# Kernel optimization log

Hardware: AMD Instinct MI355X
Metric: run time of the kernel (lower is better)

Reference implementation:

```python
import jax, jax.numpy as jnp
import numpy as np

N = 50000      # total nodes
E = 600000     # edges
F_IN = 128     # dataset.num_features
G = 500        # graphs (100 nodes each)
K = 30         # sort-pool k
D1, D2, D3 = 64, 64, 1
DTOT = D1 + D2 + D3  # 129


def gcn_conv(x, W, b, src, dst, dinv, n):
    # PyG GCNConv: x' = D^-1/2 (A+I) D^-1/2 (x W) + b ; src/dst include self-loops
    h = x @ W
    norm = dinv[src] * dinv[dst]
    msg = h[src] * norm[:, None]
    return jax.ops.segment_sum(msg, dst, num_segments=n) + b


def setup_inputs():
    key = jax.random.key(0)
    ks = jax.random.split(key, 24)
    rn = lambda k, s, sc=0.1: jax.random.normal(k, s, dtype=jnp.float32) * sc
    return {
        "x": jax.random.normal(ks[0], (N, F_IN), dtype=jnp.float32),
        "edge_index": jax.random.randint(ks[1], (2, E), 0, N),
        "W1": rn(ks[2], (F_IN, D1)), "b1": rn(ks[3], (D1,)),
        "W2": rn(ks[4], (D1, D2)),  "b2": rn(ks[5], (D2,)),
        "W3": rn(ks[6], (D2, D3)),  "b3": rn(ks[7], (D3,)),
        "Ws1": rn(ks[8], (D1, 1)),  "bs1": rn(ks[9], (1,)),
        "Ws2": rn(ks[10], (D2, 1)), "bs2": rn(ks[11], (1,)),
        "Ws3": rn(ks[12], (D3, 1)), "bs3": rn(ks[13], (1,)),
        "Wc1": rn(ks[14], (16, 1, DTOT)), "bc1": rn(ks[15], (16,)),
        "Wc2": rn(ks[16], (32, 16, 5)),   "bc2": rn(ks[17], (32,)),
        "Wl1": rn(ks[18], (128, 352)),    "bl1": rn(ks[19], (128,)),
        "Wl2": rn(ks[20], (1, 128)),      "bl2": rn(ks[21], (1,)),
        "num_graphs": G,
    }


def reference(x, edge_index, W1, b1, W2, b2, W3, b3, Ws1, bs1, Ws2, bs2, Ws3, bs3,
              Wc1, bc1, Wc2, bc2, Wl1, bl1, Wl2, bl2, num_graphs):
    n = x.shape[0]
    loops = jnp.arange(n)
    src = jnp.concatenate([edge_index[0], loops])
    dst = jnp.concatenate([edge_index[1], loops])
    deg = jnp.zeros((n,), jnp.float32).at[dst].add(1.0)
    dinv = jnp.where(deg > 0, deg ** -0.5, 0.0)

    h = jax.nn.relu(gcn_conv(x, W1, b1, src, dst, dinv, n))
    x1 = gcn_conv(h, Ws1, bs1, src, dst, dinv, n) * h
    h = jax.nn.relu(gcn_conv(h, W2, b2, src, dst, dinv, n))
    x2 = gcn_conv(h, Ws2, bs2, src, dst, dinv, n) * h
    h = jax.nn.relu(gcn_conv(h, W3, b3, src, dst, dinv, n))
    x3 = gcn_conv(h, Ws3, bs3, src, dst, dinv, n) * h
    feats = jnp.concatenate([x1, x2, x3], axis=1)  # [N, 129]

    # global_sort_pool: equal-size graphs (batch = id // npg), sort desc by last channel, keep top-K
    npg = n // num_graphs
    fg = feats.reshape(num_graphs, npg, DTOT)
    order = jnp.argsort(-fg[:, :, -1], axis=1)[:, :K]                 # [G, K]
    pooled = jnp.take_along_axis(fg, order[:, :, None], axis=1)       # [G, K, 129]

    # Conv1d(1->16, kernel=129, stride=129) == per-position dense over the 129-dim blocks
    c1 = jax.nn.relu(jnp.einsum('gkd,cd->gck', pooled, Wc1[:, 0, :]) + bc1[None, :, None])  # [G,16,30]
    mp = c1.reshape(num_graphs, 16, K // 2, 2).max(axis=-1)           # MaxPool1d(2,2) -> [G,16,15]
    c2 = jax.lax.conv_general_dilated(mp, Wc2, window_strides=(1,), padding='VALID',
                                      dimension_numbers=('NCH', 'OIH', 'NCH')) + bc2[None, :, None]
    c2 = jax.nn.relu(c2)                                              # [G,32,11]
    flat = c2.reshape(num_graphs, -1)                                 # [G,352]
    hdd = jax.nn.relu(flat @ Wl1.T + bl1)
    out = hdd @ Wl2.T + bl2
    return out[:, 0]
```

## Files before the change

kernel.cpp:

```cpp
#include <hip/hip_runtime.h>
#include <hip/hip_bf16.h>

#define NN 50000
#define EE 600000
#define FIN 128
#define GG 500
#define NPG 100
#define KK 30
#define SCHUNK 1024

__global__ void psg_deg(const int* __restrict__ dst, int* __restrict__ deg, int e) {
    int i = blockIdx.x * blockDim.x + threadIdx.x;
    if (i < e) atomicAdd(&deg[dst[i]], 1);
}

__global__ __launch_bounds__(SCHUNK) void psg_scan1(const int* __restrict__ deg,
                                                    int* __restrict__ rowptr,
                                                    int* __restrict__ csums,
                                                    float* __restrict__ dinv, int n) {
    __shared__ int sm[SCHUNK];
    int t = threadIdx.x;
    int base = blockIdx.x * SCHUNK;
    int v = (base + t < n) ? deg[base + t] : 0;
    sm[t] = v;
    __syncthreads();
    for (int off = 1; off < SCHUNK; off <<= 1) {
        int u = (t >= off) ? sm[t - off] : 0;
        __syncthreads();
        sm[t] += u;
        __syncthreads();
    }
    if (base + t < n) {
        rowptr[base + t] = sm[t] - v;
        dinv[base + t] = 1.0f / sqrtf((float)(v + 1));
    }
    if (t == SCHUNK - 1) csums[blockIdx.x] = sm[t];
}

__global__ __launch_bounds__(SCHUNK) void psg_scan3(int* __restrict__ rowptr,
                                                    int* __restrict__ rowfill,
                                                    const int* __restrict__ csums,
                                                    int n, int e) {
    __shared__ int soff;
    int t = threadIdx.x;
    if (t < 64) {
        int c = (t < (int)blockIdx.x) ? csums[t] : 0;
#pragma unroll
        for (int o = 1; o < 64; o <<= 1) c += __shfl_xor(c, o, 64);
        if (t == 0) soff = c;
    }
    __syncthreads();
    int i = blockIdx.x * SCHUNK + t;
    if (i < n) {
        int v = rowptr[i] + soff;
        rowptr[i] = v;
        rowfill[i] = v;
    }
    if (i == 0) rowptr[n] = e;
}

__global__ void psg_build(const int* __restrict__ src, const int* __restrict__ dst,
                          int* __restrict__ rowfill, int* __restrict__ csr_src, int e) {
    int i = blockIdx.x * blockDim.x + threadIdx.x;
    if (i < e) {
        int pos = atomicAdd(&rowfill[dst[i]], 1);
        csr_src[pos] = src[i];
    }
}

template <int KD>
__global__ __launch_bounds__(256) void psg_gemm(const float* __restrict__ X,
                                                const float* __restrict__ W,
                                                const float* __restrict__ dinv,
                                                float* __restrict__ hs, int n) {
    __shared__ __align__(16) float Xl[16][KD];
    __shared__ __align__(16) float WtF[(KD / 4) * 64 * 4];
    int t = threadIdx.x;
    int r0 = blockIdx.x * 16;
    for (int i = t; i < KD * 64; i += 256) {
        int k = i >> 6, j = i & 63;
        WtF[(((k >> 2) * 64 + j) << 2) + (k & 3)] = W[i];
    }
    for (int i4 = t; i4 < 16 * (KD / 4); i4 += 256) {
        int r = i4 / (KD / 4), u = i4 % (KD / 4);
        int row = r0 + r;
        float4 v = make_float4(0.f, 0.f, 0.f, 0.f);
        if (row < n) v = ((const float4*)(X + (size_t)row * KD))[u];
        ((float4*)&Xl[r][0])[u] = v;
    }
    __syncthreads();
    int j = t & 63, q = t >> 6;
    const float4* Wt4 = (const float4*)WtF;
    float a0 = 0.f, a1 = 0.f, a2 = 0.f, a3 = 0.f;
#pragma unroll 4
    for (int u = 0; u < KD / 4; ++u) {
        float4 wv = Wt4[u * 64 + j];
        float4 x0 = *(const float4*)&Xl[q * 4 + 0][u * 4];
        float4 x1 = *(const float4*)&Xl[q * 4 + 1][u * 4];
        float4 x2 = *(const float4*)&Xl[q * 4 + 2][u * 4];
        float4 x3 = *(const float4*)&Xl[q * 4 + 3][u * 4];
        a0 += x0.x * wv.x + x0.y * wv.y + x0.z * wv.z + x0.w * wv.w;
        a1 += x1.x * wv.x + x1.y * wv.y + x1.z * wv.z + x1.w * wv.w;
        a2 += x2.x * wv.x + x2.y * wv.y + x2.z * wv.z + x2.w * wv.w;
        a3 += x3.x * wv.x + x3.y * wv.y + x3.z * wv.z + x3.w * wv.w;
    }
    float av[4] = {a0, a1, a2, a3};
#pragma unroll
    for (int rr = 0; rr < 4; rr++) {
        int row = r0 + q * 4 + rr;
        if (row < n) hs[(size_t)row * 64 + j] = av[rr] * dinv[row];
    }
}

template <int NDOT>
__global__ __launch_bounds__(256) void psg_gfin(const float* __restrict__ hs,
                                                const int* __restrict__ rowptr,
                                                const int* __restrict__ csr_src,
                                                const float* __restrict__ dinv,
                                                const float* __restrict__ b,
                                                float* __restrict__ h,
                                                const float* __restrict__ wv0,
                                                float* __restrict__ s0_src,
                                                const float* __restrict__ wv1,
                                                float* __restrict__ s1_src, int n) {
    int w = (int)((blockIdx.x * 256 + threadIdx.x) >> 6);
    int j = threadIdx.x & 63;
    if (w >= n) return;
    int p0 = rowptr[w], p1 = rowptr[w + 1];
    float a0 = hs[(size_t)w * 64 + j];
    float a1 = 0.f, a2 = 0.f, a3 = 0.f, a4 = 0.f, a5 = 0.f, a6 = 0.f, a7 = 0.f;
    int p = p0;
    for (; p + 8 <= p1; p += 8) {
        int s0 = csr_src[p],     s1 = csr_src[p + 1], s2 = csr_src[p + 2], s3 = csr_src[p + 3];
        int s4 = csr_src[p + 4], s5 = csr_src[p + 5], s6 = csr_src[p + 6], s7 = csr_src[p + 7];
        a0 += hs[(size_t)s0 * 64 + j];
        a1 += hs[(size_t)s1 * 64 + j];
        a2 += hs[(size_t)s2 * 64 + j];
        a3 += hs[(size_t)s3 * 64 + j];
        a4 += hs[(size_t)s4 * 64 + j];
        a5 += hs[(size_t)s5 * 64 + j];
        a6 += hs[(size_t)s6 * 64 + j];
        a7 += hs[(size_t)s7 * 64 + j];
    }
    if (p + 4 <= p1) {
        int s0 = csr_src[p], s1 = csr_src[p + 1], s2 = csr_src[p + 2], s3 = csr_src[p + 3];
        a4 += hs[(size_t)s0 * 64 + j];
        a5 += hs[(size_t)s1 * 64 + j];
        a6 += hs[(size_t)s2 * 64 + j];
        a7 += hs[(size_t)s3 * 64 + j];
        p += 4;
    }
    for (; p < p1; ++p) a1 += hs[(size_t)csr_src[p] * 64 + j];
    float a = ((a0 + a1) + (a2 + a3)) + ((a4 + a5) + (a6 + a7));
    float di = dinv[w];
    float v = fmaxf(a * di + b[j], 0.f);
    h[(size_t)w * 64 + j] = v;
    float t0 = v * wv0[j];
#pragma unroll
    for (int o = 32; o; o >>= 1) t0 += __shfl_xor(t0, o, 64);
    if (j == 0) s0_src[w] = t0 * di;
    if (NDOT == 2) {
        float t1 = v * wv1[j];
#pragma unroll
        for (int o = 32; o; o >>= 1) t1 += __shfl_xor(t1, o, 64);
        if (j == 0) s1_src[w] = t1 * di;
    }
}

__global__ void psg_h3g(const float* __restrict__ sc_src,
                        const int* __restrict__ rowptr, const int* __restrict__ csr_src,
                        const float* __restrict__ dinv, const float* __restrict__ b3,
                        const float* __restrict__ Ws3,
                        float* __restrict__ h3, float* __restrict__ u_src, int n) {
    int i = blockIdx.x * blockDim.x + threadIdx.x;
    if (i < n) {
        float a = sc_src[i];
        int p1 = rowptr[i + 1];
        for (int p = rowptr[i]; p < p1; ++p) a += sc_src[csr_src[p]];
        float di = dinv[i];
        float v = fmaxf(a * di + b3[0], 0.f);
        h3[i] = v;
        u_src[i] = v * Ws3[0] * di;
    }
}

__device__ __forceinline__ int psg_f2ord(float f) {
    int s = __float_as_int(f);
    return s < 0 ? (s ^ 0x7fffffff) : s;
}

__global__ __launch_bounds__(128) void psg_spcnn(const float* __restrict__ u_src,
                                                 const int* __restrict__ rowptr,
                                                 const int* __restrict__ csr_src,
                                                 const float* __restrict__ dinv,
                                                 const float* __restrict__ bs1,
                                                 const float* __restrict__ bs2,
                                                 const float* __restrict__ bs3,
                                                 const float* __restrict__ sA_src,
                                                 const float* __restrict__ sB_src,
                                                 const float* __restrict__ h1,
                                                 const float* __restrict__ h2,
                                                 const float* __restrict__ h3,
                                                 const float* __restrict__ Wc1, const float* __restrict__ bc1,
                                                 const float* __restrict__ Wc2, const float* __restrict__ bc2,
                                                 const float* __restrict__ Wl1, const float* __restrict__ bl1,
                                                 const float* __restrict__ Wl2, const float* __restrict__ bl2,
                                                 float* __restrict__ out) {
    int g = blockIdx.x, t = threadIdx.x;
    __shared__ float pl[KK * 129];
    __shared__ float wc1l[16 * 129];
    __shared__ float wc2l[32 * 16 * 5];
    __shared__ float key[NPG];
    __shared__ int ord[NPG];
    __shared__ int sel[KK];
    __shared__ float sa[KK], sb[KK];
    __shared__ float c1[16 * KK];
    __shared__ float mp[16 * 15];
    __shared__ float c2s[352];
    __shared__ float hdds[128];
    __shared__ float red[2];
    for (int i = t; i < 16 * 129; i += 128) wc1l[i] = Wc1[i];
    for (int i = t; i < 32 * 16 * 5; i += 128) wc2l[i] = Wc2[i];
    if (t < NPG) {
        int node = g * NPG + t;
        float a = u_src[node];
        int pe = rowptr[node + 1];
        for (int p = rowptr[node]; p < pe; ++p) a += u_src[csr_src[p]];
        float v = (a * dinv[node] + bs3[0]) * h3[node];
        key[t] = v;
        ord[t] = psg_f2ord(v);
    }
    __syncthreads();
    if (t < NPG) {
        int v = ord[t];
        int r = 0;
        for (int m = 0; m < NPG; m++) {
            int u = ord[m];
            r += (u > v) || (u == v && m < t);
        }
        if (r < KK) sel[r] = t;
    }
    __syncthreads();
    {
        int r = t & 31;
        if (t < 64 && r < KK) {
            int node = g * NPG + sel[r];
            const float* ssrc = (t < 32) ? sA_src : sB_src;
            float a = ssrc[node];
            int pe = rowptr[node + 1];
            for (int p = rowptr[node]; p < pe; ++p) a += ssrc[csr_src[p]];
            float scl = a * dinv[node] + ((t < 32) ? bs1[0] : bs2[0]);
            if (t < 32) sa[r] = scl; else sb[r] = scl;
        }
    }
    __syncthreads();
    for (int idx = t; idx < KK * 129; idx += 128) {
        int r = idx / 129, c = idx - r * 129;
        int node = g * NPG + sel[r];
        float v;
        if (c < 64) v = sa[r] * h1[(size_t)node * 64 + c];
        else if (c < 128) v = sb[r] * h2[(size_t)node * 64 + (c - 64)];
        else v = key[sel[r]];
        pl[idx] = v;
    }
    __syncthreads();
    for (int idx = t; idx < 16 * KK; idx += 128) {
        int c = idx / KK, k = idx % KK;
        float a = bc1[c];
        for (int d = 0; d < 129; d++) a += pl[k * 129 + d] * wc1l[c * 129 + d];
        c1[c * KK + k] = fmaxf(a, 0.f);
    }
    __syncthreads();
    for (int idx = t; idx < 16 * 15; idx += 128) {
        int c = idx / 15, k = idx % 15;
        mp[idx] = fmaxf(c1[c * KK + 2 * k], c1[c * KK + 2 * k + 1]);
    }
    __syncthreads();
    for (int idx = t; idx < 352; idx += 128) {
        int o = idx / 11, k = idx % 11;
        float a = bc2[o];
        for (int i2 = 0; i2 < 16; i2++) {
#pragma unroll
            for (int k2 = 0; k2 < 5; k2++) a += mp[i2 * 15 + k + k2] * wc2l[(o * 16 + i2) * 5 + k2];
        }
        c2s[o * 11 + k] = fmaxf(a, 0.f);
    }
    __syncthreads();
    {
        float a = bl1[t];
        const float* wr = Wl1 + (size_t)t * 352;
        for (int f = 0; f < 352; f++) a += c2s[f] * wr[f];
        hdds[t] = fmaxf(a, 0.f);
    }
    __syncthreads();
    float p = hdds[t] * Wl2[t];
#pragma unroll
    for (int o = 32; o; o >>= 1) p += __shfl_xor(p, o, 64);
    if ((t & 63) == 0) red[t >> 6] = p;
    __syncthreads();
    if (t == 0) out[g] = red[0] + red[1] + bl2[0];
}

extern "C" void kernel_launch(void* const* d_in, const int* in_sizes, int n_in,
                              void* d_out, int out_size, void* d_ws, size_t ws_size,
                              hipStream_t stream) {
    const float* x   = (const float*)d_in[0];
    const int*   ei  = (const int*)d_in[1];
    const float* W1  = (const float*)d_in[2];
    const float* b1  = (const float*)d_in[3];
    const float* W2  = (const float*)d_in[4];
    const float* b2  = (const float*)d_in[5];
    const float* W3  = (const float*)d_in[6];
    const float* b3  = (const float*)d_in[7];
    const float* Ws1 = (const float*)d_in[8];
    const float* bs1 = (const float*)d_in[9];
    const float* Ws2 = (const float*)d_in[10];
    const float* bs2 = (const float*)d_in[11];
    const float* Ws3 = (const float*)d_in[12];
    const float* bs3 = (const float*)d_in[13];
    const float* Wc1 = (const float*)d_in[14];
    const float* bc1 = (const float*)d_in[15];
    const float* Wc2 = (const float*)d_in[16];
    const float* bc2 = (const float*)d_in[17];
    const float* Wl1 = (const float*)d_in[18];
    const float* bl1 = (const float*)d_in[19];
    const float* Wl2 = (const float*)d_in[20];
    const float* bl2 = (const float*)d_in[21];
    float* out = (float*)d_out;

    const int n = in_sizes[0] / FIN;
    const int e = in_sizes[1] / 2;
    const int* src = ei;
    const int* dst = ei + e;
    const int nchunk = (n + SCHUNK - 1) / SCHUNK;

    char* w = (char*)d_ws;
    float* dinv    = (float*)w; w += (size_t)n * 4;
    float* sA_src  = (float*)w; w += (size_t)n * 4;
    float* sB_src  = (float*)w; w += (size_t)n * 4;
    float* sC_src  = (float*)w; w += (size_t)n * 4;
    float* h3      = (float*)w; w += (size_t)n * 4;
    float* u_src   = (float*)w; w += (size_t)n * 4;
    int*   deg     = (int*)w;   w += (size_t)n * 4;
    int*   rowptr  = (int*)w;   w += (size_t)(n + 1) * 4;
    int*   rowfill = (int*)w;   w += (size_t)n * 4;
    int*   csums   = (int*)w;   w += 64 * 4;
    int*   csr_src = (int*)w;   w += (size_t)e * 4;
    float* hs      = (float*)w; w += (size_t)n * 64 * 4;
    float* h1      = (float*)w; w += (size_t)n * 64 * 4;
    float* h2      = (float*)w; w += (size_t)n * 64 * 4;

    const int nb_e  = (e + 255) / 256;
    const int nb_n  = (n + 255) / 256;
    const int nb_g  = (n + 15) / 16;
    const int nb_nw = (n * 64 + 255) / 256;

    hipMemsetAsync(deg, 0, (size_t)n * 4, stream);
    psg_deg<<<nb_e, 256, 0, stream>>>(dst, deg, e);
    psg_scan1<<<nchunk, SCHUNK, 0, stream>>>(deg, rowptr, csums, dinv, n);
    psg_scan3<<<nchunk, SCHUNK, 0, stream>>>(rowptr, rowfill, csums, n, e);
    psg_build<<<nb_e, 256, 0, stream>>>(src, dst, rowfill, csr_src, e);

    psg_gemm<128><<<nb_g, 256, 0, stream>>>(x, W1, dinv, hs, n);
    psg_gfin<1><<<nb_nw, 256, 0, stream>>>(hs, rowptr, csr_src, dinv, b1, h1,
                                           Ws1, sA_src, nullptr, nullptr, n);

    psg_gemm<64><<<nb_g, 256, 0, stream>>>(h1, W2, dinv, hs, n);
    psg_gfin<2><<<nb_nw, 256, 0, stream>>>(hs, rowptr, csr_src, dinv, b2, h2,
                                           Ws2, sB_src, W3, sC_src, n);

    psg_h3g<<<nb_n, 256, 0, stream>>>(sC_src, rowptr, csr_src, dinv, b3, Ws3, h3, u_src, n);

    psg_spcnn<<<GG, 128, 0, stream>>>(u_src, rowptr, csr_src, dinv, bs1, bs2, bs3,
                                      sA_src, sB_src, h1, h2, h3,
                                      Wc1, bc1, Wc2, bc2, Wl1, bl1, Wl2, bl2, out);

    (void)n_in; (void)out_size; (void)ws_size;
}
```

Before: 346.2 us.

## Move per-node scalar gathers out of sort-pool kernel into full-grid passes

```diff
diff --git a/kernel.cpp b/kernel.cpp
--- a/kernel.cpp
+++ b/kernel.cpp
@@ -167,20 +167,44 @@
     }
 }
 
-__global__ void psg_h3g(const float* __restrict__ sc_src,
+__global__ void psg_h3g(const float* __restrict__ sC_src,
+                        const float* __restrict__ sA_src,
+                        const float* __restrict__ sB_src,
                         const int* __restrict__ rowptr, const int* __restrict__ csr_src,
                         const float* __restrict__ dinv, const float* __restrict__ b3,
                         const float* __restrict__ Ws3,
-                        float* __restrict__ h3, float* __restrict__ u_src, int n) {
+                        const float* __restrict__ bs1, const float* __restrict__ bs2,
+                        float* __restrict__ h3, float* __restrict__ u_src,
+                        float* __restrict__ xs1, float* __restrict__ xs2, int n) {
     int i = blockIdx.x * blockDim.x + threadIdx.x;
     if (i < n) {
-        float a = sc_src[i];
+        float aC = sC_src[i], aA = sA_src[i], aB = sB_src[i];
         int p1 = rowptr[i + 1];
-        for (int p = rowptr[i]; p < p1; ++p) a += sc_src[csr_src[p]];
+        for (int p = rowptr[i]; p < p1; ++p) {
+            int s = csr_src[p];
+            aC += sC_src[s];
+            aA += sA_src[s];
+            aB += sB_src[s];
+        }
         float di = dinv[i];
-        float v = fmaxf(a * di + b3[0], 0.f);
+        float v = fmaxf(aC * di + b3[0], 0.f);
         h3[i] = v;
         u_src[i] = v * Ws3[0] * di;
+        xs1[i] = aA * di + bs1[0];
+        xs2[i] = aB * di + bs2[0];
+    }
+}
+
+__global__ void psg_x3g(const float* __restrict__ u_src,
+                        const int* __restrict__ rowptr, const int* __restrict__ csr_src,
+                        const float* __restrict__ dinv, const float* __restrict__ bs3,
+                        const float* __restrict__ h3, float* __restrict__ x3, int n) {
+    int i = blockIdx.x * blockDim.x + threadIdx.x;
+    if (i < n) {
+        float a = u_src[i];
+        int p1 = rowptr[i + 1];
+        for (int p = rowptr[i]; p < p1; ++p) a += u_src[csr_src[p]];
+        x3[i] = (a * dinv[i] + bs3[0]) * h3[i];
     }
 }
 
@@ -189,18 +213,11 @@
     return s < 0 ? (s ^ 0x7fffffff) : s;
 }
 
-__global__ __launch_bounds__(128) void psg_spcnn(const float* __restrict__ u_src,
-                                                 const int* __restrict__ rowptr,
-                                                 const int* __restrict__ csr_src,
-                                                 const float* __restrict__ dinv,
-                                                 const float* __restrict__ bs1,
-                                                 const float* __restrict__ bs2,
-                                                 const float* __restrict__ bs3,
-                                                 const float* __restrict__ sA_src,
-                                                 const float* __restrict__ sB_src,
+__global__ __launch_bounds__(256) void psg_spcnn(const float* __restrict__ x3,
+                                                 const float* __restrict__ xs1,
+                                                 const float* __restrict__ xs2,
                                                  const float* __restrict__ h1,
                                                  const float* __restrict__ h2,
-                                                 const float* __restrict__ h3,
                                                  const float* __restrict__ Wc1, const float* __restrict__ bc1,
                                                  const float* __restrict__ Wc2, const float* __restrict__ bc2,
                                                  const float* __restrict__ Wl1, const float* __restrict__ bl1,
@@ -219,14 +236,10 @@
     __shared__ float c2s[352];
     __shared__ float hdds[128];
     __shared__ float red[2];
-    for (int i = t; i < 16 * 129; i += 128) wc1l[i] = Wc1[i];
-    for (int i = t; i < 32 * 16 * 5; i += 128) wc2l[i] = Wc2[i];
+    for (int i = t; i < 16 * 129; i += 256) wc1l[i] = Wc1[i];
+    for (int i = t; i < 32 * 16 * 5; i += 256) wc2l[i] = Wc2[i];
     if (t < NPG) {
-        int node = g * NPG + t;
-        float a = u_src[node];
-        int pe = rowptr[node + 1];
-        for (int p = rowptr[node]; p < pe; ++p) a += u_src[csr_src[p]];
-        float v = (a * dinv[node] + bs3[0]) * h3[node];
+        float v = x3[g * NPG + t];
         key[t] = v;
         ord[t] = psg_f2ord(v);
     }
@@ -241,20 +254,10 @@
         if (r < KK) sel[r] = t;
     }
     __syncthreads();
-    {
-        int r = t & 31;
-        if (t < 64 && r < KK) {
-            int node = g * NPG + sel[r];
-            const float* ssrc = (t < 32) ? sA_src : sB_src;
-            float a = ssrc[node];
-            int pe = rowptr[node + 1];
-            for (int p = rowptr[node]; p < pe; ++p) a += ssrc[csr_src[p]];
-            float scl = a * dinv[node] + ((t < 32) ? bs1[0] : bs2[0]);
-            if (t < 32) sa[r] = scl; else sb[r] = scl;
-        }
-    }
-    __syncthreads();
-    for (int idx = t; idx < KK * 129; idx += 128) {
+    if (t < KK) sa[t] = xs1[g * NPG + sel[t]];
+    else if (t >= 32 && t < 32 + KK) sb[t - 32] = xs2[g * NPG + sel[t - 32]];
+    __syncthreads();
+    for (int idx = t; idx < KK * 129; idx += 256) {
         int r = idx / 129, c = idx - r * 129;
         int node = g * NPG + sel[r];
         float v;
@@ -264,19 +267,19 @@
         pl[idx] = v;
     }
     __syncthreads();
-    for (int idx = t; idx < 16 * KK; idx += 128) {
+    for (int idx = t; idx < 16 * KK; idx += 256) {
         int c = idx / KK, k = idx % KK;
         float a = bc1[c];
         for (int d = 0; d < 129; d++) a += pl[k * 129 + d] * wc1l[c * 129 + d];
         c1[c * KK + k] = fmaxf(a, 0.f);
     }
     __syncthreads();
-    for (int idx = t; idx < 16 * 15; idx += 128) {
+    for (int idx = t; idx < 16 * 15; idx += 256) {
         int c = idx / 15, k = idx % 15;
         mp[idx] = fmaxf(c1[c * KK + 2 * k], c1[c * KK + 2 * k + 1]);
     }
     __syncthreads();
-    for (int idx = t; idx < 352; idx += 128) {
+    for (int idx = t; idx < 352; idx += 256) {
         int o = idx / 11, k = idx % 11;
         float a = bc2[o];
         for (int i2 = 0; i2 < 16; i2++) {
@@ -286,17 +289,19 @@
         c2s[o * 11 + k] = fmaxf(a, 0.f);
     }
     __syncthreads();
-    {
+    if (t < 128) {
         float a = bl1[t];
         const float* wr = Wl1 + (size_t)t * 352;
         for (int f = 0; f < 352; f++) a += c2s[f] * wr[f];
         hdds[t] = fmaxf(a, 0.f);
     }
     __syncthreads();
-    float p = hdds[t] * Wl2[t];
-#pragma unroll
-    for (int o = 32; o; o >>= 1) p += __shfl_xor(p, o, 64);
-    if ((t & 63) == 0) red[t >> 6] = p;
+    if (t < 128) {
+        float p = hdds[t] * Wl2[t];
+#pragma unroll
+        for (int o = 32; o; o >>= 1) p += __shfl_xor(p, o, 64);
+        if ((t & 63) == 0) red[t >> 6] = p;
+    }
     __syncthreads();
     if (t == 0) out[g] = red[0] + red[1] + bl2[0];
 }
@@ -341,6 +346,9 @@
     float* sC_src  = (float*)w; w += (size_t)n * 4;
     float* h3      = (float*)w; w += (size_t)n * 4;
     float* u_src   = (float*)w; w += (size_t)n * 4;
+    float* xs1     = (float*)w; w += (size_t)n * 4;
+    float* xs2     = (float*)w; w += (size_t)n * 4;
+    float* x3      = (float*)w; w += (size_t)n * 4;
     int*   deg     = (int*)w;   w += (size_t)n * 4;
     int*   rowptr  = (int*)w;   w += (size_t)(n + 1) * 4;
     int*   rowfill = (int*)w;   w += (size_t)n * 4;
@@ -369,10 +377,11 @@
     psg_gfin<2><<<nb_nw, 256, 0, stream>>>(hs, rowptr, csr_src, dinv, b2, h2,
                                            Ws2, sB_src, W3, sC_src, n);
 
-    psg_h3g<<<nb_n, 256, 0, stream>>>(sC_src, rowptr, csr_src, dinv, b3, Ws3, h3, u_src, n);
-
-    psg_spcnn<<<GG, 128, 0, stream>>>(u_src, rowptr, csr_src, dinv, bs1, bs2, bs3,
-                                      sA_src, sB_src, h1, h2, h3,
+    psg_h3g<<<nb_n, 256, 0, stream>>>(sC_src, sA_src, sB_src, rowptr, csr_src, dinv,
+                                      b3, Ws3, bs1, bs2, h3, u_src, xs1, xs2, n);
+    psg_x3g<<<nb_n, 256, 0, stream>>>(u_src, rowptr, csr_src, dinv, bs3, h3, x3, n);
+
+    psg_spcnn<<<GG, 256, 0, stream>>>(x3, xs1, xs2, h1, h2,
                                       Wc1, bc1, Wc2, bc2, Wl1, bl1, Wl2, bl2, out);
 
     (void)n_in; (void)out_size; (void)ws_size;
```

Result: no change. 345.7 us (-0.1%).
